# Kernel tuning notes

Measured on AMD Instinct MI355X. Metric: run time of the kernel, lower is better.

Reference implementation:

```python
import itertools
import jax, jax.numpy as jnp
import numpy as np

B, N, C, O = 8, 32, 64, 64
PERMS = list(itertools.permutations((1, 2, 3)))  # build_idx_3_permutations order


def _lin(k, fan_in, out, lead=()):
    # torch nn.Linear default init: U(-1/sqrt(fan_in), 1/sqrt(fan_in)) for W and b
    kw, kb = jax.random.split(k)
    bound = 1.0 / float(np.sqrt(fan_in))
    W = jax.random.uniform(kw, lead + (fan_in, out), minval=-bound, maxval=bound, dtype=jnp.float32)
    b = jax.random.uniform(kb, lead + (out,), minval=-bound, maxval=bound, dtype=jnp.float32)
    return W, b


def setup_inputs() -> dict:
    key = jax.random.key(0)
    ks = jax.random.split(key, 8)
    x = jax.random.normal(ks[0], (B, N, N, N, C), dtype=jnp.float32)
    W33, b33 = _lin(ks[1], 6 * C, O)            # three_to_three linear
    W22, b22 = _lin(ks[2], 12 * C, O, (3,))     # two_to_two (a2 cat transpose), 3 diagonal planes
    W12, b12 = _lin(ks[3], 10 * C, O, (3,))     # one_to_two
    W12t, b12t = _lin(ks[4], 10 * C, O, (3,))   # one_to_two_t
    W02, b02 = _lin(ks[5], 5 * C, O, (3,))      # zero_to_two
    W11, b11 = _lin(ks[6], 10 * C, O)           # one_to_one (in_node_channels = 0)
    W01, b01 = _lin(ks[7], 5 * C, O)            # zero_to_one
    return dict(x=x, W33=W33, b33=b33, W22=W22, b22=b22, W12=W12, b12=b12,
                W12t=W12t, b12t=b12t, W02=W02, b02=b02, W11=W11, b11=b11,
                W01=W01, b01=b01)


def _contractions(x):
    """All second/first/zeroth-order mean contractions of x: [B,n,n,n,C]."""
    s1, s2, s3 = x.mean(1), x.mean(2), x.mean(3)                      # [B,n,n,C]
    # diagonals arranged as [B, other_axis, diag_axis, C]
    d12 = jnp.moveaxis(jnp.diagonal(x, axis1=1, axis2=2), -1, 2)      # [B,n3,diag,C]
    d13 = jnp.moveaxis(jnp.diagonal(x, axis1=1, axis2=3), -1, 2)      # [B,n2,diag,C]
    d23 = jnp.moveaxis(jnp.diagonal(x, axis1=2, axis2=3), -1, 2)      # [B,n1,diag,C]
    a2 = jnp.concatenate([s1, s2, s3, d12, d13, d23], axis=-1)        # [B,n,n,6C]
    tdiag = jnp.moveaxis(jnp.diagonal(d23, axis1=1, axis2=2), -1, 1)  # [B,n,C] triple diagonal x[b,i,i,i]
    a1 = jnp.concatenate([
        x.mean((1, 2)), x.mean((1, 3)), x.mean((2, 3)),               # double sums
        d12.mean(1), d12.mean(2), d13.mean(1), d13.mean(2),           # diag sums
        d23.mean(1), d23.mean(2),
        tdiag], axis=-1)                                              # [B,n,10C]
    a0 = jnp.concatenate([
        x.mean((1, 2, 3)),                                            # triple sum
        d12.mean((1, 2)), d13.mean((1, 2)), d23.mean((1, 2)),         # diag-sum-sum
        tdiag.mean(1)], axis=-1)                                      # [B,5C]
    return a2, a1, a0


def reference(x, W33, b33, W22, b22, W12, b12, W12t, b12t, W02, b02, W11, b11, W01, b01):
    n = x.shape[1]
    a2, a1, a0 = _contractions(x)
    # third-order mix: concat all 6 spatial permutations, then linear 6C -> O
    allp = jnp.concatenate([jnp.transpose(x, (0,) + p + (4,)) for p in PERMS], axis=-1)
    T = allp @ W33 + b33                                              # [B,n,n,n,O]
    # second-order mixes for the 3 diagonal planes
    a2wt = jnp.concatenate([a2, jnp.swapaxes(a2, 1, 2)], axis=-1)     # [B,n,n,12C]
    slices = []
    for i in range(3):
        m = a2wt @ W22[i] + b22[i]
        m = m + (a1 @ W12[i] + b12[i])[:, :, None, :]
        m = m + (a1 @ W12t[i] + b12t[i])[:, None, :, :]
        m = m + (a0 @ W02[i] + b02[i])[:, None, None, :]
        slices.append(m)                                              # [B,n(other),n(diag),O]
    # first-order (core-diagonal) mix
    mdiag = a1 @ W11 + b11 + (a0 @ W01 + b01)[:, None, :]             # [B,n,O]
    # _expand_mix: accumulate slices onto diagonal planes of T (diagonal_free=False)
    idx = jnp.arange(n)
    # plane (1,2): T[b,d,d,t] += slices[0][b,t,d]
    T = T.at[:, idx, idx].add(jnp.swapaxes(slices[0], 1, 2))
    # plane (1,3): T[b,d,t,d] += slices[1][b,t,d]
    Tsw = jnp.swapaxes(T, 2, 3)
    Tsw = Tsw.at[:, idx, idx].add(jnp.swapaxes(slices[1], 1, 2))
    T = jnp.swapaxes(Tsw, 2, 3)
    # plane (2,3): T[b,t,d,d] += slices[2][b,t,d]
    T = T.at[:, :, idx, idx].add(slices[2])
    # triple diagonal: T[b,d,d,d] += mdiag[b,d]
    T = T.at[:, idx, idx, idx].add(mdiag)
    return T
```

## Files before the change

kernel.cpp:

```cpp
#include <hip/hip_runtime.h>

#define NBATCH 8
#define NN 32
#define NC 64
#define NO 64
#define C6 384
#define C10 640
#define C12 768
#define C5 320

typedef __attribute__((ext_vector_type(8))) short short8;
typedef __attribute__((ext_vector_type(4))) float float4v;

static constexpr int OFF_ABF = 0;
static constexpr int OFF_A1  = 1572864;
static constexpr int OFF_A0  = 1736704;
static constexpr int OFF_R1  = 1739264;
static constexpr int OFF_R1T = 1788416;
static constexpr int OFF_R0  = 1837568;
static constexpr int OFF_MD  = 1839104;
static constexpr int OFF_WB  = 1855488;
static constexpr int OFF_WB2 = 1867776;

__device__ __forceinline__ unsigned short f2bf(float f) {
    union { float f; unsigned u; } x{f};
    unsigned r = x.u + 0x7fffu + ((x.u >> 16) & 1u);
    return (unsigned short)(r >> 16);
}

__device__ __forceinline__ void store_bf4(unsigned short* p, float4v v) {
    ushort4 w;
    w.x = f2bf(v.x); w.y = f2bf(v.y); w.z = f2bf(v.z); w.w = f2bf(v.w);
    *(ushort4*)p = w;
}

__device__ __forceinline__ float4v bf4(const unsigned short* p) {
    ushort4 u = *(const ushort4*)(p);
    float4v r;
    r.x = __uint_as_float((unsigned)u.x << 16);
    r.y = __uint_as_float((unsigned)u.y << 16);
    r.z = __uint_as_float((unsigned)u.z << 16);
    r.w = __uint_as_float((unsigned)u.w << 16);
    return r;
}

__global__ __launch_bounds__(256) void k_prepw(const float* __restrict__ W33,
                                               const float* __restrict__ W22,
                                               float* __restrict__ ws) {
    int id = blockIdx.x * 256 + threadIdx.x;
    if (id < 3072) {
        int lane = id & 63;
        int ks = (id >> 6) % 12;
        int nt = (id >> 6) / 12;
        int n = nt * 16 + (lane & 15);
        int k0 = ks * 32 + (lane >> 4) * 8;
        unsigned short* dst = (unsigned short*)(ws + OFF_WB) +
                              (size_t)((nt * 12 + ks) * 64 + lane) * 8;
#pragma unroll
        for (int jj = 0; jj < 8; ++jj) dst[jj] = f2bf(W33[(k0 + jj) * 64 + n]);
    } else if (id < 21504) {
        int q = id - 3072;
        int lane = q & 63;
        int ks = (q >> 6) % 24;
        int r = (q >> 6) / 24;
        int nt = r & 3;
        int i = r >> 2;
        int n = nt * 16 + (lane & 15);
        int k0 = ks * 32 + (lane >> 4) * 8;
        const float* W = W22 + (size_t)i * C12 * NO;
        unsigned short* dst = (unsigned short*)(ws + OFF_WB2) +
                              (size_t)(((i * 4 + nt) * 24 + ks) * 64 + lane) * 8;
#pragma unroll
        for (int jj = 0; jj < 8; ++jj) dst[jj] = f2bf(W[(k0 + jj) * 64 + n]);
    }
}

__global__ __launch_bounds__(256) void k_contract2(const float* __restrict__ x,
                                                   float* __restrict__ ws) {
    int id = blockIdx.x * 256 + threadIdx.x;
    int c4 = id & 15;
    int v = (id >> 4) & 31;
    int u = (id >> 9) & 31;
    int b = id >> 14;
    int bc = c4 * 4;
    const float* xb = x + (size_t)b * 2097152;

    float4v s1 = {0.f, 0.f, 0.f, 0.f}, s2 = s1, s3 = s1;
    {
        const float* p = xb + u * 2048 + v * 64 + bc;
        for (int i = 0; i < 32; ++i) s1 += *(const float4v*)(p + i * 65536);
    }
    {
        const float* p = xb + u * 65536 + v * 64 + bc;
        for (int j = 0; j < 32; ++j) s2 += *(const float4v*)(p + j * 2048);
    }
    {
        const float* p = xb + u * 65536 + v * 2048 + bc;
        for (int k = 0; k < 32; ++k) s3 += *(const float4v*)(p + k * 64);
    }
    float4v d12 = *(const float4v*)(xb + v * 65536 + v * 2048 + u * 64 + bc);
    float4v d13 = *(const float4v*)(xb + v * 65536 + u * 2048 + v * 64 + bc);
    float4v d23 = *(const float4v*)(xb + u * 65536 + v * 2048 + v * 64 + bc);

    const float inv = 1.0f / 32.0f;
    unsigned short* a2 = (unsigned short*)(ws + OFF_ABF) +
                         (size_t)((b * 32 + u) * 32 + v) * C6 + bc;
    store_bf4(a2 + 0 * 64, s1 * inv);
    store_bf4(a2 + 1 * 64, s2 * inv);
    store_bf4(a2 + 2 * 64, s3 * inv);
    store_bf4(a2 + 3 * 64, d12);
    store_bf4(a2 + 4 * 64, d13);
    store_bf4(a2 + 5 * 64, d23);
}

__global__ __launch_bounds__(256) void k_contract1(const float* __restrict__ x,
                                                   float* __restrict__ ws) {
    int id = blockIdx.x * 256 + threadIdx.x;
    int c4 = id & 15;
    int t = (id >> 4) & 31;
    int b = id >> 9;
    int bc = c4 * 4;
    const unsigned short* a2 = (const unsigned short*)(ws + OFF_ABF) +
                               (size_t)b * 32 * 32 * C6;

    float4v su0 = {0.f,0.f,0.f,0.f}, su3 = su0, su4 = su0, su5 = su0;
    float4v sv0 = su0, sv1 = su0, sv3 = su0, sv4 = su0, sv5 = su0;
    for (int u = 0; u < 32; ++u) {
        const unsigned short* row = a2 + (size_t)(u * 32 + t) * C6 + bc;
        su0 += bf4(row + 0);
        su3 += bf4(row + 192);
        su4 += bf4(row + 256);
        su5 += bf4(row + 320);
    }
    for (int v = 0; v < 32; ++v) {
        const unsigned short* row = a2 + (size_t)(t * 32 + v) * C6 + bc;
        sv0 += bf4(row + 0);
        sv1 += bf4(row + 64);
        sv3 += bf4(row + 192);
        sv4 += bf4(row + 256);
        sv5 += bf4(row + 320);
    }
    float4v td = *(const float4v*)(x + (((size_t)b * 32 + t) * 32 + t) * 2048 + t * 64 + bc);

    float* a1 = ws + OFF_A1 + ((size_t)b * 32 + t) * C10;
    const float inv = 1.0f / 32.0f;
    *(float4v*)(a1 + 0 * 64 + bc) = su0 * inv;
    *(float4v*)(a1 + 1 * 64 + bc) = sv0 * inv;
    *(float4v*)(a1 + 2 * 64 + bc) = sv1 * inv;
    *(float4v*)(a1 + 3 * 64 + bc) = su3 * inv;
    *(float4v*)(a1 + 4 * 64 + bc) = sv3 * inv;
    *(float4v*)(a1 + 5 * 64 + bc) = su4 * inv;
    *(float4v*)(a1 + 6 * 64 + bc) = sv4 * inv;
    *(float4v*)(a1 + 7 * 64 + bc) = su5 * inv;
    *(float4v*)(a1 + 8 * 64 + bc) = sv5 * inv;
    *(float4v*)(a1 + 9 * 64 + bc) = td;
}

__global__ __launch_bounds__(256) void k_contract0(float* __restrict__ ws) {
    int id = blockIdx.x * 256 + threadIdx.x;
    if (id >= 512) return;
    int c = id & 63;
    int b = id >> 6;
    const float* a1 = ws + OFF_A1 + (size_t)b * 32 * C10;
    float s0 = 0, s1 = 0, s2 = 0, s3 = 0, s4 = 0;
    for (int t = 0; t < 32; ++t) {
        const float* row = a1 + t * C10;
        s0 += row[0 * 64 + c];
        s1 += row[3 * 64 + c];
        s2 += row[5 * 64 + c];
        s3 += row[7 * 64 + c];
        s4 += row[9 * 64 + c];
    }
    float* a0 = ws + OFF_A0 + b * C5;
    const float inv = 1.0f / 32.0f;
    a0[0 * 64 + c] = s0 * inv;
    a0[1 * 64 + c] = s1 * inv;
    a0[2 * 64 + c] = s2 * inv;
    a0[3 * 64 + c] = s3 * inv;
    a0[4 * 64 + c] = s4 * inv;
}

__global__ __launch_bounds__(256) void k_rowmix(
    const float* __restrict__ W12, const float* __restrict__ b12,
    const float* __restrict__ W12t, const float* __restrict__ b12t,
    const float* __restrict__ W02, const float* __restrict__ b02,
    const float* __restrict__ W11, const float* __restrict__ b11,
    const float* __restrict__ W01, const float* __restrict__ b01,
    float* __restrict__ ws) {
    int id = blockIdx.x * 256 + threadIdx.x;
    if (id < 98304) {
        bool second = id >= 49152;
        int q = second ? id - 49152 : id;
        int o = q & 63;
        int t = (q >> 6) & 31;
        int b = (q >> 11) & 7;
        int i = q >> 14;
        const float* W = (second ? W12t : W12) + (size_t)i * C10 * NO;
        const float* bb = (second ? b12t : b12) + i * NO;
        const float* a1 = ws + OFF_A1 + ((size_t)b * 32 + t) * C10;
        float acc = bb[o];
        for (int m = 0; m < C10; ++m) acc += a1[m] * W[m * NO + o];
        ws[(second ? OFF_R1T : OFF_R1) + (((size_t)i * 8 + b) * 32 + t) * NO + o] = acc;
    } else if (id < 114688) {
        int q = id - 98304;
        int o = q & 63;
        int t = (q >> 6) & 31;
        int b = q >> 11;
        const float* a1 = ws + OFF_A1 + ((size_t)b * 32 + t) * C10;
        const float* a0 = ws + OFF_A0 + (size_t)b * C5;
        float acc = b11[o] + b01[o];
        for (int m = 0; m < C10; ++m) acc += a1[m] * W11[m * NO + o];
        for (int m = 0; m < C5; ++m) acc += a0[m] * W01[m * NO + o];
        ws[OFF_MD + ((size_t)b * 32 + t) * NO + o] = acc;
    } else if (id < 116224) {
        int q = id - 114688;
        int o = q & 63;
        int b = (q >> 6) & 7;
        int i = q >> 9;
        const float* a0 = ws + OFF_A0 + (size_t)b * C5;
        float acc = b02[i * NO + o];
        for (int m = 0; m < C5; ++m) acc += a0[m] * W02[(size_t)i * C5 * NO + m * NO + o];
        ws[OFF_R0 + ((size_t)i * 8 + b) * NO + o] = acc;
    }
}

__global__ __launch_bounds__(256) void k_main(const float* __restrict__ x,
                                              const float* __restrict__ ws,
                                              const float* __restrict__ b33,
                                              float* __restrict__ T) {
    __shared__ __align__(16) unsigned short As[32 * 392];
    int tid = threadIdx.x;
    const unsigned short* WB = (const unsigned short*)(ws + OFF_WB);

    int wv = tid >> 6;
    int lane = tid & 63;
    int m_tile = wv & 1;
    int n_pair = wv >> 1;
    int colq = lane & 15;
    int quad = lane >> 4;

    short8 bfr[2][12];
#pragma unroll
    for (int np = 0; np < 2; ++np) {
        int nt = n_pair * 2 + np;
#pragma unroll
        for (int ks = 0; ks < 12; ++ks)
            bfr[np][ks] = *(const short8*)(WB + (size_t)((nt * 12 + ks) * 64 + lane) * 8);
    }
    float bb0 = b33[(n_pair * 2 + 0) * 16 + colq];
    float bb1 = b33[(n_pair * 2 + 1) * 16 + colq];

    int k0 = wv * 8;
    int c = colq * 4;
    int mrow = m_tile * 16 + colq;
    const unsigned short* Arow = &As[mrow * 392 + quad * 8];

    for (int tile = blockIdx.x; tile < 8192; tile += 2048) {
        int b = tile >> 10;
        int i = (tile >> 5) & 31;
        int j = tile & 31;
        const float* xb = x + (size_t)b * 2097152;

#pragma unroll
        for (int half = 0; half < 2; ++half) {
            int k = k0 + quad + half * 4;
            float4v v0 = *(const float4v*)(xb + i * 65536 + j * 2048 + k * 64 + c);
            float4v v1 = *(const float4v*)(xb + i * 65536 + k * 2048 + j * 64 + c);
            float4v v2 = *(const float4v*)(xb + j * 65536 + i * 2048 + k * 64 + c);
            float4v v3 = *(const float4v*)(xb + k * 65536 + i * 2048 + j * 64 + c);
            float4v v4 = *(const float4v*)(xb + j * 65536 + k * 2048 + i * 64 + c);
            float4v v5 = *(const float4v*)(xb + k * 65536 + j * 2048 + i * 64 + c);
            unsigned short* dst = &As[k * 392 + c];
            store_bf4(dst + 0 * 64, v0);
            store_bf4(dst + 1 * 64, v1);
            store_bf4(dst + 2 * 64, v2);
            store_bf4(dst + 3 * 64, v3);
            store_bf4(dst + 4 * 64, v4);
            store_bf4(dst + 5 * 64, v5);
        }
        __syncthreads();

        float4v acc0 = {0.f, 0.f, 0.f, 0.f};
        float4v acc1 = {0.f, 0.f, 0.f, 0.f};
#pragma unroll
        for (int ks = 0; ks < 12; ++ks) {
            short8 a = *(const short8*)(Arow + ks * 32);
            acc0 = __builtin_amdgcn_mfma_f32_16x16x32_bf16(a, bfr[0][ks], acc0, 0, 0, 0);
            acc1 = __builtin_amdgcn_mfma_f32_16x16x32_bf16(a, bfr[1][ks], acc1, 0, 0, 0);
        }

        float* Tb = T + (size_t)tile * 2048;
#pragma unroll
        for (int r = 0; r < 4; ++r) {
            int m = m_tile * 16 + quad * 4 + r;
            int o0 = (n_pair * 2 + 0) * 16 + colq;
            int o1 = (n_pair * 2 + 1) * 16 + colq;
            __builtin_nontemporal_store(acc0[r] + bb0, &Tb[m * 64 + o0]);
            __builtin_nontemporal_store(acc1[r] + bb1, &Tb[m * 64 + o1]);
        }
        __syncthreads();
    }
}

__global__ __launch_bounds__(256) void k_slices(const float* __restrict__ b22,
                                                float* __restrict__ T,
                                                const float* __restrict__ ws) {
    __shared__ __align__(16) unsigned short As[32 * 776];
    int blk = blockIdx.x;
    int b = blk >> 5;
    int t = blk & 31;
    int tid = threadIdx.x;
    const unsigned short* abf = (const unsigned short*)(ws + OFF_ABF);
    const unsigned short* WB2 = (const unsigned short*)(ws + OFF_WB2);

    for (int l = tid; l < 3072; l += 256) {
        int d = l / 96;
        int m8 = l - d * 96;
        const unsigned short* src = (m8 < 48)
            ? abf + (size_t)(((b * 32 + t) * 32 + d) * C6) + m8 * 8
            : abf + (size_t)(((b * 32 + d) * 32 + t) * C6) + (m8 - 48) * 8;
        *(short8*)&As[d * 776 + m8 * 8] = *(const short8*)src;
    }
    __syncthreads();

    int wv = tid >> 6;
    int lane = tid & 63;
    int mt = wv & 1;
    int nh = wv >> 1;
    float4v zero = {0.f, 0.f, 0.f, 0.f};
    float4v acc[3][2] = {{zero, zero}, {zero, zero}, {zero, zero}};
    const unsigned short* Arow = &As[(mt * 16 + (lane & 15)) * 776 + (lane >> 4) * 8];
#pragma unroll
    for (int ks = 0; ks < 24; ++ks) {
        short8 a = *(const short8*)(Arow + ks * 32);
#pragma unroll
        for (int i = 0; i < 3; ++i) {
#pragma unroll
            for (int np = 0; np < 2; ++np) {
                int nt = nh * 2 + np;
                short8 bf = *(const short8*)(WB2 + (size_t)(((i * 4 + nt) * 24 + ks) * 64 + lane) * 8);
                acc[i][np] = __builtin_amdgcn_mfma_f32_16x16x32_bf16(a, bf, acc[i][np], 0, 0, 0);
            }
        }
    }

    int colq = lane & 15;
    int quad = lane >> 4;
    float* Tb = T + (size_t)b * 2097152;
#pragma unroll
    for (int np = 0; np < 2; ++np) {
        int o = (nh * 2 + np) * 16 + colq;
        float base0 = b22[0 * 64 + o] + ws[OFF_R1 + ((size_t)(0 * 8 + b) * 32 + t) * 64 + o]
                    + ws[OFF_R0 + (size_t)(0 * 8 + b) * 64 + o];
        float base1 = b22[1 * 64 + o] + ws[OFF_R1 + ((size_t)(1 * 8 + b) * 32 + t) * 64 + o]
                    + ws[OFF_R0 + (size_t)(1 * 8 + b) * 64 + o];
        float base2 = b22[2 * 64 + o] + ws[OFF_R1 + ((size_t)(2 * 8 + b) * 32 + t) * 64 + o]
                    + ws[OFF_R0 + (size_t)(2 * 8 + b) * 64 + o];
#pragma unroll
        for (int r = 0; r < 4; ++r) {
            int d = mt * 16 + quad * 4 + r;
            float s0 = acc[0][np][r] + base0 + ws[OFF_R1T + ((size_t)(0 * 8 + b) * 32 + d) * 64 + o];
            float s1 = acc[1][np][r] + base1 + ws[OFF_R1T + ((size_t)(1 * 8 + b) * 32 + d) * 64 + o];
            float s2 = acc[2][np][r] + base2 + ws[OFF_R1T + ((size_t)(2 * 8 + b) * 32 + d) * 64 + o];
            if (d != t) {
                Tb[d * 65536 + d * 2048 + t * 64 + o] += s0;
                Tb[d * 65536 + t * 2048 + d * 64 + o] += s1;
                Tb[t * 65536 + d * 2048 + d * 64 + o] += s2;
            } else {
                float md = ws[OFF_MD + ((size_t)b * 32 + d) * 64 + o];
                Tb[d * 65536 + d * 2048 + d * 64 + o] += s0 + s1 + s2 + md;
            }
        }
    }
}

extern "C" void kernel_launch(void* const* d_in, const int* in_sizes, int n_in,
                              void* d_out, int out_size, void* d_ws, size_t ws_size,
                              hipStream_t stream) {
    const float* x    = (const float*)d_in[0];
    const float* W33  = (const float*)d_in[1];
    const float* b33  = (const float*)d_in[2];
    const float* W22  = (const float*)d_in[3];
    const float* b22  = (const float*)d_in[4];
    const float* W12  = (const float*)d_in[5];
    const float* b12  = (const float*)d_in[6];
    const float* W12t = (const float*)d_in[7];
    const float* b12t = (const float*)d_in[8];
    const float* W02  = (const float*)d_in[9];
    const float* b02  = (const float*)d_in[10];
    const float* W11  = (const float*)d_in[11];
    const float* b11  = (const float*)d_in[12];
    const float* W01  = (const float*)d_in[13];
    const float* b01  = (const float*)d_in[14];
    float* T  = (float*)d_out;
    float* ws = (float*)d_ws;

    hipLaunchKernelGGL(k_prepw, dim3(84), dim3(256), 0, stream, W33, W22, ws);
    hipLaunchKernelGGL(k_contract2, dim3(512), dim3(256), 0, stream, x, ws);
    hipLaunchKernelGGL(k_contract1, dim3(16), dim3(256), 0, stream, x, ws);
    hipLaunchKernelGGL(k_contract0, dim3(2), dim3(256), 0, stream, ws);
    hipLaunchKernelGGL(k_rowmix, dim3(454), dim3(256), 0, stream,
                       W12, b12, W12t, b12t, W02, b02, W11, b11, W01, b01, ws);
    hipLaunchKernelGGL(k_main, dim3(2048), dim3(256), 0, stream, x, ws, b33, T);
    hipLaunchKernelGGL(k_slices, dim3(256), dim3(256), 0, stream, b22, T, ws);
}
```

Before: 288.4 us.

## Parallelize contract1 and rowmix reductions, prefetch next tile in main GEMM

k_contract1 now spreads each (b,t) reduction across a 256-thread block with shared-memory partial sums instead of 16 blocks doing serial 32-step loops. k_rowmix gives each (b,t) its own block, computing all seven row mixes with the a1 load shared and the K dimension split across four groups, then reduced in shared memory. k_main assigns each block four consecutive j tiles and software-prefetches the next tile's x loads into registers while the MFMA and store of the current tile run. These changes target low parallelism in the small kernels and load latency in the main kernel, at the cost of more registers in k_main.

```diff
diff --git a/kernel.cpp b/kernel.cpp
--- a/kernel.cpp
+++ b/kernel.cpp
@@ -115,45 +115,52 @@
 
 __global__ __launch_bounds__(256) void k_contract1(const float* __restrict__ x,
                                                    float* __restrict__ ws) {
-    int id = blockIdx.x * 256 + threadIdx.x;
-    int c4 = id & 15;
-    int t = (id >> 4) & 31;
-    int b = id >> 9;
+    __shared__ float4v P[9][16][16];
+    int blk = blockIdx.x;
+    int b = blk >> 5;
+    int t = blk & 31;
+    int tid = threadIdx.x;
+    int g = tid >> 4;
+    int c4 = tid & 15;
     int bc = c4 * 4;
     const unsigned short* a2 = (const unsigned short*)(ws + OFF_ABF) +
                                (size_t)b * 32 * 32 * C6;
 
-    float4v su0 = {0.f,0.f,0.f,0.f}, su3 = su0, su4 = su0, su5 = su0;
-    float4v sv0 = su0, sv1 = su0, sv3 = su0, sv4 = su0, sv5 = su0;
-    for (int u = 0; u < 32; ++u) {
-        const unsigned short* row = a2 + (size_t)(u * 32 + t) * C6 + bc;
-        su0 += bf4(row + 0);
-        su3 += bf4(row + 192);
-        su4 += bf4(row + 256);
-        su5 += bf4(row + 320);
-    }
-    for (int v = 0; v < 32; ++v) {
-        const unsigned short* row = a2 + (size_t)(t * 32 + v) * C6 + bc;
-        sv0 += bf4(row + 0);
-        sv1 += bf4(row + 64);
-        sv3 += bf4(row + 192);
-        sv4 += bf4(row + 256);
-        sv5 += bf4(row + 320);
-    }
-    float4v td = *(const float4v*)(x + (((size_t)b * 32 + t) * 32 + t) * 2048 + t * 64 + bc);
+    float4v p0 = {0.f,0.f,0.f,0.f}, p1 = p0, p2 = p0, p3 = p0, p4 = p0,
+            p5 = p0, p6 = p0, p7 = p0, p8 = p0;
+#pragma unroll
+    for (int w = 0; w < 2; ++w) {
+        int u = 2 * g + w;
+        const unsigned short* rowu = a2 + (size_t)(u * 32 + t) * C6 + bc;
+        p0 += bf4(rowu + 0);
+        p3 += bf4(rowu + 192);
+        p5 += bf4(rowu + 256);
+        p7 += bf4(rowu + 320);
+        const unsigned short* rowv = a2 + (size_t)(t * 32 + u) * C6 + bc;
+        p1 += bf4(rowv + 0);
+        p2 += bf4(rowv + 64);
+        p4 += bf4(rowv + 192);
+        p6 += bf4(rowv + 256);
+        p8 += bf4(rowv + 320);
+    }
+    P[0][g][c4] = p0; P[1][g][c4] = p1; P[2][g][c4] = p2;
+    P[3][g][c4] = p3; P[4][g][c4] = p4; P[5][g][c4] = p5;
+    P[6][g][c4] = p6; P[7][g][c4] = p7; P[8][g][c4] = p8;
+    __syncthreads();
 
     float* a1 = ws + OFF_A1 + ((size_t)b * 32 + t) * C10;
-    const float inv = 1.0f / 32.0f;
-    *(float4v*)(a1 + 0 * 64 + bc) = su0 * inv;
-    *(float4v*)(a1 + 1 * 64 + bc) = sv0 * inv;
-    *(float4v*)(a1 + 2 * 64 + bc) = sv1 * inv;
-    *(float4v*)(a1 + 3 * 64 + bc) = su3 * inv;
-    *(float4v*)(a1 + 4 * 64 + bc) = sv3 * inv;
-    *(float4v*)(a1 + 5 * 64 + bc) = su4 * inv;
-    *(float4v*)(a1 + 6 * 64 + bc) = sv4 * inv;
-    *(float4v*)(a1 + 7 * 64 + bc) = su5 * inv;
-    *(float4v*)(a1 + 8 * 64 + bc) = sv5 * inv;
-    *(float4v*)(a1 + 9 * 64 + bc) = td;
+    if (tid < 144) {
+        int p = tid >> 4;
+        int cc = tid & 15;
+        float4v s = {0.f,0.f,0.f,0.f};
+#pragma unroll
+        for (int gg = 0; gg < 16; ++gg) s += P[p][gg][cc];
+        *(float4v*)(a1 + p * 64 + cc * 4) = s * (1.0f / 32.0f);
+    } else if (tid < 160) {
+        int cc = tid - 144;
+        float4v td = *(const float4v*)(x + (((size_t)b * 32 + t) * 32 + t) * 2048 + t * 64 + cc * 4);
+        *(float4v*)(a1 + 9 * 64 + cc * 4) = td;
+    }
 }
 
 __global__ __launch_bounds__(256) void k_contract0(float* __restrict__ ws) {
@@ -187,40 +194,59 @@
     const float* __restrict__ W11, const float* __restrict__ b11,
     const float* __restrict__ W01, const float* __restrict__ b01,
     float* __restrict__ ws) {
-    int id = blockIdx.x * 256 + threadIdx.x;
-    if (id < 98304) {
-        bool second = id >= 49152;
-        int q = second ? id - 49152 : id;
-        int o = q & 63;
-        int t = (q >> 6) & 31;
-        int b = (q >> 11) & 7;
-        int i = q >> 14;
-        const float* W = (second ? W12t : W12) + (size_t)i * C10 * NO;
-        const float* bb = (second ? b12t : b12) + i * NO;
-        const float* a1 = ws + OFF_A1 + ((size_t)b * 32 + t) * C10;
-        float acc = bb[o];
-        for (int m = 0; m < C10; ++m) acc += a1[m] * W[m * NO + o];
-        ws[(second ? OFF_R1T : OFF_R1) + (((size_t)i * 8 + b) * 32 + t) * NO + o] = acc;
-    } else if (id < 114688) {
-        int q = id - 98304;
-        int o = q & 63;
-        int t = (q >> 6) & 31;
-        int b = q >> 11;
+    int blk = blockIdx.x;
+    int tid = threadIdx.x;
+    if (blk < 256) {
+        __shared__ float P2[7][4][64];
+        int b = blk >> 5;
+        int t = blk & 31;
+        int o = tid & 63;
+        int g = tid >> 6;
         const float* a1 = ws + OFF_A1 + ((size_t)b * 32 + t) * C10;
         const float* a0 = ws + OFF_A0 + (size_t)b * C5;
-        float acc = b11[o] + b01[o];
-        for (int m = 0; m < C10; ++m) acc += a1[m] * W11[m * NO + o];
-        for (int m = 0; m < C5; ++m) acc += a0[m] * W01[m * NO + o];
-        ws[OFF_MD + ((size_t)b * 32 + t) * NO + o] = acc;
-    } else if (id < 116224) {
-        int q = id - 114688;
-        int o = q & 63;
-        int b = (q >> 6) & 7;
-        int i = q >> 9;
-        const float* a0 = ws + OFF_A0 + (size_t)b * C5;
-        float acc = b02[i * NO + o];
-        for (int m = 0; m < C5; ++m) acc += a0[m] * W02[(size_t)i * C5 * NO + m * NO + o];
-        ws[OFF_R0 + ((size_t)i * 8 + b) * NO + o] = acc;
+        float acc[7] = {0.f, 0.f, 0.f, 0.f, 0.f, 0.f, 0.f};
+        for (int m = g * 160; m < g * 160 + 160; ++m) {
+            float a = a1[m];
+            acc[0] += a * W12 [(size_t)0 * C10 * NO + m * NO + o];
+            acc[1] += a * W12 [(size_t)1 * C10 * NO + m * NO + o];
+            acc[2] += a * W12 [(size_t)2 * C10 * NO + m * NO + o];
+            acc[3] += a * W12t[(size_t)0 * C10 * NO + m * NO + o];
+            acc[4] += a * W12t[(size_t)1 * C10 * NO + m * NO + o];
+            acc[5] += a * W12t[(size_t)2 * C10 * NO + m * NO + o];
+            acc[6] += a * W11 [m * NO + o];
+        }
+        for (int m = g * 80; m < g * 80 + 80; ++m)
+            acc[6] += a0[m] * W01[m * NO + o];
+#pragma unroll
+        for (int kk = 0; kk < 7; ++kk) P2[kk][g][o] = acc[kk];
+        __syncthreads();
+        for (int out = tid; out < 448; out += 256) {
+            int kind = out >> 6;
+            int oo = out & 63;
+            float s = P2[kind][0][oo] + P2[kind][1][oo] + P2[kind][2][oo] + P2[kind][3][oo];
+            if (kind < 3) {
+                s += b12[kind * NO + oo];
+                ws[OFF_R1 + (((size_t)kind * 8 + b) * 32 + t) * NO + oo] = s;
+            } else if (kind < 6) {
+                int i = kind - 3;
+                s += b12t[i * NO + oo];
+                ws[OFF_R1T + (((size_t)i * 8 + b) * 32 + t) * NO + oo] = s;
+            } else {
+                s += b11[oo] + b01[oo];
+                ws[OFF_MD + ((size_t)b * 32 + t) * NO + oo] = s;
+            }
+        }
+    } else {
+        for (int idx = tid; idx < 1536; idx += 256) {
+            int i = idx >> 9;
+            int b = (idx >> 6) & 7;
+            int o = idx & 63;
+            const float* a0 = ws + OFF_A0 + (size_t)b * C5;
+            float acc = b02[i * NO + o];
+            for (int m = 0; m < C5; ++m)
+                acc += a0[m] * W02[(size_t)i * C5 * NO + m * NO + o];
+            ws[OFF_R0 + ((size_t)i * 8 + b) * NO + o] = acc;
+        }
     }
 }
 
@@ -250,35 +276,58 @@
     float bb0 = b33[(n_pair * 2 + 0) * 16 + colq];
     float bb1 = b33[(n_pair * 2 + 1) * 16 + colq];
 
+    int blk = blockIdx.x;
+    int b = blk >> 8;
+    int i = (blk >> 3) & 31;
+    int jg = blk & 7;
+    const float* xb = x + (size_t)b * 2097152;
+
     int k0 = wv * 8;
     int c = colq * 4;
+    int kA = k0 + quad;
+    int kB = k0 + quad + 4;
     int mrow = m_tile * 16 + colq;
     const unsigned short* Arow = &As[mrow * 392 + quad * 8];
 
-    for (int tile = blockIdx.x; tile < 8192; tile += 2048) {
-        int b = tile >> 10;
-        int i = (tile >> 5) & 31;
-        int j = tile & 31;
-        const float* xb = x + (size_t)b * 2097152;
-
-#pragma unroll
-        for (int half = 0; half < 2; ++half) {
-            int k = k0 + quad + half * 4;
-            float4v v0 = *(const float4v*)(xb + i * 65536 + j * 2048 + k * 64 + c);
-            float4v v1 = *(const float4v*)(xb + i * 65536 + k * 2048 + j * 64 + c);
-            float4v v2 = *(const float4v*)(xb + j * 65536 + i * 2048 + k * 64 + c);
-            float4v v3 = *(const float4v*)(xb + k * 65536 + i * 2048 + j * 64 + c);
-            float4v v4 = *(const float4v*)(xb + j * 65536 + k * 2048 + i * 64 + c);
-            float4v v5 = *(const float4v*)(xb + k * 65536 + j * 2048 + i * 64 + c);
-            unsigned short* dst = &As[k * 392 + c];
-            store_bf4(dst + 0 * 64, v0);
-            store_bf4(dst + 1 * 64, v1);
-            store_bf4(dst + 2 * 64, v2);
-            store_bf4(dst + 3 * 64, v3);
-            store_bf4(dst + 4 * 64, v4);
-            store_bf4(dst + 5 * 64, v5);
-        }
+    auto load_tile = [&](int j, float4v* pf) {
+        pf[0]  = *(const float4v*)(xb + i * 65536 + j * 2048 + kA * 64 + c);
+        pf[1]  = *(const float4v*)(xb + i * 65536 + kA * 2048 + j * 64 + c);
+        pf[2]  = *(const float4v*)(xb + j * 65536 + i * 2048 + kA * 64 + c);
+        pf[3]  = *(const float4v*)(xb + kA * 65536 + i * 2048 + j * 64 + c);
+        pf[4]  = *(const float4v*)(xb + j * 65536 + kA * 2048 + i * 64 + c);
+        pf[5]  = *(const float4v*)(xb + kA * 65536 + j * 2048 + i * 64 + c);
+        pf[6]  = *(const float4v*)(xb + i * 65536 + j * 2048 + kB * 64 + c);
+        pf[7]  = *(const float4v*)(xb + i * 65536 + kB * 2048 + j * 64 + c);
+        pf[8]  = *(const float4v*)(xb + j * 65536 + i * 2048 + kB * 64 + c);
+        pf[9]  = *(const float4v*)(xb + kB * 65536 + i * 2048 + j * 64 + c);
+        pf[10] = *(const float4v*)(xb + j * 65536 + kB * 2048 + i * 64 + c);
+        pf[11] = *(const float4v*)(xb + kB * 65536 + j * 2048 + i * 64 + c);
+    };
+
+    float4v pf[12];
+    load_tile(jg * 4, pf);
+
+#pragma unroll
+    for (int s = 0; s < 4; ++s) {
+        int j = jg * 4 + s;
+        unsigned short* dA = &As[kA * 392 + c];
+        store_bf4(dA + 0 * 64, pf[0]);
+        store_bf4(dA + 1 * 64, pf[1]);
+        store_bf4(dA + 2 * 64, pf[2]);
+        store_bf4(dA + 3 * 64, pf[3]);
+        store_bf4(dA + 4 * 64, pf[4]);
+        store_bf4(dA + 5 * 64, pf[5]);
+        unsigned short* dB = &As[kB * 392 + c];
+        store_bf4(dB + 0 * 64, pf[6]);
+        store_bf4(dB + 1 * 64, pf[7]);
+        store_bf4(dB + 2 * 64, pf[8]);
+        store_bf4(dB + 3 * 64, pf[9]);
+        store_bf4(dB + 4 * 64, pf[10]);
+        store_bf4(dB + 5 * 64, pf[11]);
         __syncthreads();
+
+        float4v nf[12];
+        if (s < 3) load_tile(j + 1, nf);
 
         float4v acc0 = {0.f, 0.f, 0.f, 0.f};
         float4v acc1 = {0.f, 0.f, 0.f, 0.f};
@@ -289,7 +338,7 @@
             acc1 = __builtin_amdgcn_mfma_f32_16x16x32_bf16(a, bfr[1][ks], acc1, 0, 0, 0);
         }
 
-        float* Tb = T + (size_t)tile * 2048;
+        float* Tb = T + ((size_t)(b * 1024 + i * 32 + j)) * 2048;
 #pragma unroll
         for (int r = 0; r < 4; ++r) {
             int m = m_tile * 16 + quad * 4 + r;
@@ -299,6 +348,10 @@
             __builtin_nontemporal_store(acc1[r] + bb1, &Tb[m * 64 + o1]);
         }
         __syncthreads();
+        if (s < 3) {
+#pragma unroll
+            for (int q = 0; q < 12; ++q) pf[q] = nf[q];
+        }
     }
 }
 
@@ -397,9 +450,9 @@
 
     hipLaunchKernelGGL(k_prepw, dim3(84), dim3(256), 0, stream, W33, W22, ws);
     hipLaunchKernelGGL(k_contract2, dim3(512), dim3(256), 0, stream, x, ws);
-    hipLaunchKernelGGL(k_contract1, dim3(16), dim3(256), 0, stream, x, ws);
+    hipLaunchKernelGGL(k_contract1, dim3(256), dim3(256), 0, stream, x, ws);
     hipLaunchKernelGGL(k_contract0, dim3(2), dim3(256), 0, stream, ws);
-    hipLaunchKernelGGL(k_rowmix, dim3(454), dim3(256), 0, stream,
+    hipLaunchKernelGGL(k_rowmix, dim3(257), dim3(256), 0, stream,
                        W12, b12, W12t, b12t, W02, b02, W11, b11, W01, b01, ws);
     hipLaunchKernelGGL(k_main, dim3(2048), dim3(256), 0, stream, x, ws, b33, T);
     hipLaunchKernelGGL(k_slices, dim3(256), dim3(256), 0, stream, b22, T, ws);
```

After: 293.6 us. No clear change (+1.8%).
